# Kernel optimization log

Measured on AMD Instinct MI355X. Metric: run time of the kernel, lower is better.

Reference implementation:

```python
import jax, jax.numpy as jnp
import numpy as np
from functools import partial

B, T, D, H, V, L, NL = 2, 2048, 512, 8, 32000, 4, 3
HID = 4 * D
HD = D // H
EPS = 1e-5


def layernorm(x, g, b):
    mu = jnp.mean(x, axis=-1, keepdims=True)
    var = jnp.mean(jnp.square(x - mu), axis=-1, keepdims=True)
    return (x - mu) * jax.lax.rsqrt(var + EPS) * g + b


def self_mod_attn(x, Wq, Wk, Wv, Wo):
    # x: [B,T,D]; W*: [D,D] (applied as x @ W)
    def heads(w):
        return jnp.transpose((x @ w).reshape(B, T, H, HD), (1, 0, 2, 3))  # [T,B,H,HD]
    q, k, v = heads(Wq), heads(Wk), heads(Wv)

    def step(mem, qkv):
        q_t, k_t, v_t = qkv  # each [B,H,HD]
        mem = mem + jnp.einsum('bhd,bhk->hdk', v_t, k_t) / B  # batch-mean outer product
        y_t = jnp.einsum('hdk,bhk->bhd', mem, q_t)
        return mem, y_t

    mem0 = jnp.zeros((H, HD, HD), dtype=x.dtype)
    _, ys = jax.lax.scan(step, mem0, (q, k, v))  # ys: [T,B,H,HD]
    out = jnp.transpose(ys, (1, 0, 2, 3)).reshape(B, T, D)
    return out @ Wo


def cms(x, W1, b1, W2, b2):
    # Continuum memory system: NL parallel MLP levels (dim -> 4*dim -> dim, GELU), averaged.
    h = jax.nn.gelu(jnp.einsum('btd,ndh->nbth', x, W1) + b1[:, None, None, :])
    y = jnp.einsum('nbth,nhd->nbtd', h, W2) + b2[:, None, None, :]
    return jnp.mean(y, axis=0)


def setup_inputs() -> dict:
    key = jax.random.key(0)
    ks = jax.random.split(key, 16)
    std = 0.02
    p = {
        'emb': jax.random.normal(ks[0], (V, D), jnp.float32) * std,
        'pos': jax.random.normal(ks[1], (2048, D), jnp.float32) * std,
        'ln1_g': jnp.ones((L, D)), 'ln1_b': jnp.zeros((L, D)),
        'Wq': jax.random.normal(ks[2], (L, D, D), jnp.float32) * std,
        'Wk': jax.random.normal(ks[3], (L, D, D), jnp.float32) * std,
        'Wv': jax.random.normal(ks[4], (L, D, D), jnp.float32) * std,
        'Wo': jax.random.normal(ks[5], (L, D, D), jnp.float32) * std,
        'ln2_g': jnp.ones((L, D)), 'ln2_b': jnp.zeros((L, D)),
        'cms_W1': jax.random.normal(ks[6], (L, NL, D, HID), jnp.float32) * std,
        'cms_b1': jnp.zeros((L, NL, HID)),
        'cms_W2': jax.random.normal(ks[7], (L, NL, HID, D), jnp.float32) * std,
        'cms_b2': jnp.zeros((L, NL, D)),
        'lnf_g': jnp.ones((D,)), 'lnf_b': jnp.zeros((D,)),
        'input_ids': jax.random.randint(ks[8], (B, T), 0, V, jnp.int32),
    }
    return p


def reference(emb, pos, ln1_g, ln1_b, Wq, Wk, Wv, Wo, ln2_g, ln2_b,
              cms_W1, cms_b1, cms_W2, cms_b2, lnf_g, lnf_b, input_ids):
    x = emb[input_ids] + pos[:T][None, :, :]  # [B,T,D]
    for l in range(L):
        x = x + self_mod_attn(layernorm(x, ln1_g[l], ln1_b[l]), Wq[l], Wk[l], Wv[l], Wo[l])
        x = x + cms(layernorm(x, ln2_g[l], ln2_b[l]), cms_W1[l], cms_b1[l], cms_W2[l], cms_b2[l])
    x = layernorm(x, lnf_g, lnf_b)
    logits = x @ emb.T  # tied head, [B,T,V]
    return logits
```

## Files before the change

kernel.cpp:

```cpp
#include <hip/hip_runtime.h>
#include <stdint.h>

#define B_ 2
#define T_ 2048
#define D_ 512
#define H_ 8
#define HD_ 64
#define V_ 32000
#define L_ 4
#define NL_ 3
#define HID_ 2048
#define NROW 4096
#define CCH 64
#define CROWS 128
#define NC 32
#define EPS_ 1e-5f

typedef __attribute__((ext_vector_type(8))) __bf16 bf16x8;
typedef __attribute__((ext_vector_type(4))) float f32x4;

__device__ __forceinline__ float b2f(unsigned short u) {
  union { uint32_t i; float f; } v; v.i = ((uint32_t)u) << 16; return v.f;
}
__device__ __forceinline__ unsigned short f2b(float f) {
  union { float f; uint32_t i; } v; v.f = f;
  uint32_t u = v.i;
  u += 0x7fffu + ((u >> 16) & 1u);
  return (unsigned short)(u >> 16);
}

__global__ __launch_bounds__(256) void k_prep(
    const float* __restrict__ emb, const float* __restrict__ pos,
    const int* __restrict__ ids,
    const float* __restrict__ Wq, const float* __restrict__ Wk,
    const float* __restrict__ Wv, const float* __restrict__ Wo,
    const float* __restrict__ W1, const float* __restrict__ W2,
    const float* __restrict__ b2,
    const float* __restrict__ ln1g, const float* __restrict__ ln1b,
    unsigned short* __restrict__ WqkvT, unsigned short* __restrict__ WoT,
    unsigned short* __restrict__ W1T, unsigned short* __restrict__ W2cat,
    unsigned short* __restrict__ embB, float* __restrict__ bsum,
    float* __restrict__ x, unsigned short* __restrict__ h) {
  int bid = blockIdx.x, tid = threadIdx.x;
  __shared__ float tile[32][33];
  __shared__ float red[4], red2[4];
  int tx = tid & 31, ty = tid >> 5;
  if (bid < 4096) {
    int z = bid >> 8, r = bid & 255;
    int bx = (r & 15) * 32, by = (r >> 4) * 32;
    const float* in; unsigned short* out;
    if (z < 12) {
      int l = z / 3, m = z - l * 3;
      in = (m == 0 ? Wq : m == 1 ? Wk : Wv) + (size_t)l * D_ * D_;
      out = WqkvT + (size_t)z * D_ * D_;
    } else {
      in = Wo + (size_t)(z - 12) * D_ * D_;
      out = WoT + (size_t)(z - 12) * D_ * D_;
    }
#pragma unroll
    for (int i = 0; i < 4; i++)
      tile[ty + 8 * i][tx] = in[(size_t)(by + ty + 8 * i) * D_ + bx + tx];
    __syncthreads();
#pragma unroll
    for (int i = 0; i < 4; i++)
      out[(size_t)(bx + ty + 8 * i) * D_ + by + tx] = f2b(tile[tx][ty + 8 * i]);
  } else if (bid < 16384) {
    int s = bid - 4096;
    int z = s >> 10, r = s & 1023;
    int bx = (r & 63) * 32, by = (r >> 6) * 32;
    const float* in = W1 + (size_t)z * D_ * HID_;
    unsigned short* out = W1T + (size_t)z * HID_ * D_;
#pragma unroll
    for (int i = 0; i < 4; i++)
      tile[ty + 8 * i][tx] = in[(size_t)(by + ty + 8 * i) * HID_ + bx + tx];
    __syncthreads();
#pragma unroll
    for (int i = 0; i < 4; i++)
      out[(size_t)(bx + ty + 8 * i) * D_ + by + tx] = f2b(tile[tx][ty + 8 * i]);
  } else if (bid < 28672) {
    int s = bid - 16384;
    int z = s >> 10, r = s & 1023;
    int l = z / 3, n = z - l * 3;
    int bx = (r & 15) * 32, by = (r >> 4) * 32;
    const float* in = W2 + (size_t)z * HID_ * D_;
#pragma unroll
    for (int i = 0; i < 4; i++)
      tile[ty + 8 * i][tx] = in[(size_t)(by + ty + 8 * i) * D_ + bx + tx];
    __syncthreads();
#pragma unroll
    for (int i = 0; i < 4; i++)
      W2cat[((size_t)l * D_ + bx + ty + 8 * i) * (NL_ * HID_) + n * HID_ + by + tx] =
          f2b(tile[tx][ty + 8 * i]);
  } else if (bid < 44672) {
    int s = bid - 28672;
    int base = (s * 256 + tid) * 4;
    float4 v = *(const float4*)(emb + base);
    unsigned short o[4] = { f2b(v.x), f2b(v.y), f2b(v.z), f2b(v.w) };
    *(uint2*)(embB + base) = *(const uint2*)o;
  } else if (bid < 46720) {
    int s = bid - 44672;
    int i = s * 256 + tid;
    int row = i >> 7, cg = i & 127;
    int t = row & (T_ - 1);
    int id = ids[row];
    float4 e = ((const float4*)(emb + (size_t)id * D_))[cg];
    float4 p = ((const float4*)(pos + (size_t)t * D_))[cg];
    float4 xv; xv.x = e.x + p.x; xv.y = e.y + p.y; xv.z = e.z + p.z; xv.w = e.w + p.w;
    ((float4*)(x + (size_t)row * D_))[cg] = xv;
    float sum = xv.x + xv.y + xv.z + xv.w;
#pragma unroll
    for (int o = 32; o >= 1; o >>= 1) sum += __shfl_xor(sum, o);
    int wv = tid >> 6;
    if ((tid & 63) == 0) red[wv] = sum;
    __syncthreads();
    int wb = (tid >> 7) * 2;
    float mu = (red[wb] + red[wb + 1]) * (1.f / D_);
    float dx = xv.x - mu, dy = xv.y - mu, dz = xv.z - mu, dw = xv.w - mu;
    float s2 = dx * dx + dy * dy + dz * dz + dw * dw;
#pragma unroll
    for (int o = 32; o >= 1; o >>= 1) s2 += __shfl_xor(s2, o);
    if ((tid & 63) == 0) red2[wv] = s2;
    __syncthreads();
    float var = (red2[wb] + red2[wb + 1]) * (1.f / D_);
    float rs = rsqrtf(var + EPS_);
    float4 gv = ((const float4*)ln1g)[cg];
    float4 bv = ((const float4*)ln1b)[cg];
    unsigned short o4[4] = { f2b(dx * rs * gv.x + bv.x), f2b(dy * rs * gv.y + bv.y),
                             f2b(dz * rs * gv.z + bv.z), f2b(dw * rs * gv.w + bv.w) };
    *(uint2*)(h + (size_t)row * D_ + cg * 4) = *(const uint2*)o4;
  } else {
    int s = bid - 46720;
    int l = s >> 1, d = (s & 1) * 256 + tid;
    float acc = 0.f;
#pragma unroll
    for (int n = 0; n < NL_; n++) acc += b2[((size_t)l * NL_ + n) * D_ + d];
    bsum[(size_t)l * D_ + d] = acc;
  }
}

__global__ __launch_bounds__(128) void k_ln(
    const float* __restrict__ x, const float* __restrict__ g,
    const float* __restrict__ b, unsigned short* __restrict__ out) {
  int row = blockIdx.x;
  int tid = threadIdx.x;
  const float* xr = x + (size_t)row * D_;
  float4 v = ((const float4*)xr)[tid];
  float s = v.x + v.y + v.z + v.w;
#pragma unroll
  for (int o = 32; o >= 1; o >>= 1) s += __shfl_xor(s, o);
  __shared__ float red[2], red2[2];
  int wv = tid >> 6;
  if ((tid & 63) == 0) red[wv] = s;
  __syncthreads();
  float mu = (red[0] + red[1]) * (1.f / D_);
  float dx = v.x - mu, dy = v.y - mu, dz = v.z - mu, dw = v.w - mu;
  float s2 = dx * dx + dy * dy + dz * dz + dw * dw;
#pragma unroll
  for (int o = 32; o >= 1; o >>= 1) s2 += __shfl_xor(s2, o);
  if ((tid & 63) == 0) red2[wv] = s2;
  __syncthreads();
  float var = (red2[0] + red2[1]) * (1.f / D_);
  float rs = rsqrtf(var + EPS_);
  float4 gv = ((const float4*)g)[tid];
  float4 bv = ((const float4*)b)[tid];
  unsigned short o4[4] = { f2b(dx * rs * gv.x + bv.x), f2b(dy * rs * gv.y + bv.y),
                           f2b(dz * rs * gv.z + bv.z), f2b(dw * rs * gv.w + bv.w) };
  *(uint2*)(out + (size_t)row * D_ + tid * 4) = *(const uint2*)o4;
}

__global__ __launch_bounds__(256) void k_cmsred_ln(
    float* __restrict__ x, const float* __restrict__ parts,
    const float* __restrict__ bsum, const float* __restrict__ g,
    const float* __restrict__ b, unsigned short* __restrict__ h) {
  int bid = blockIdx.x, tid = threadIdx.x;
  int row = bid * 2 + (tid >> 7);
  int cg = tid & 127;
  size_t base = (size_t)row * D_ + cg * 4;
  float4 xv = *(const float4*)(x + base);
  float4 p0 = *(const float4*)(parts + base);
  float4 p1 = *(const float4*)(parts + (size_t)NROW * D_ + base);
  float4 p2 = *(const float4*)(parts + 2ull * NROW * D_ + base);
  float4 bs = *(const float4*)(bsum + cg * 4);
  const float k3 = 1.f / 3.f;
  xv.x += (p0.x + p1.x + p2.x + bs.x) * k3;
  xv.y += (p0.y + p1.y + p2.y + bs.y) * k3;
  xv.z += (p0.z + p1.z + p2.z + bs.z) * k3;
  xv.w += (p0.w + p1.w + p2.w + bs.w) * k3;
  *(float4*)(x + base) = xv;
  float sum = xv.x + xv.y + xv.z + xv.w;
#pragma unroll
  for (int o = 32; o >= 1; o >>= 1) sum += __shfl_xor(sum, o);
  __shared__ float red[4], red2[4];
  int wv = tid >> 6;
  if ((tid & 63) == 0) red[wv] = sum;
  __syncthreads();
  int wb = (tid >> 7) * 2;
  float mu = (red[wb] + red[wb + 1]) * (1.f / D_);
  float dx = xv.x - mu, dy = xv.y - mu, dz = xv.z - mu, dw = xv.w - mu;
  float s2 = dx * dx + dy * dy + dz * dz + dw * dw;
#pragma unroll
  for (int o = 32; o >= 1; o >>= 1) s2 += __shfl_xor(s2, o);
  if ((tid & 63) == 0) red2[wv] = s2;
  __syncthreads();
  float var = (red2[wb] + red2[wb + 1]) * (1.f / D_);
  float rs = rsqrtf(var + EPS_);
  float4 gv = ((const float4*)g)[cg];
  float4 bv = ((const float4*)b)[cg];
  unsigned short o4[4] = { f2b(dx * rs * gv.x + bv.x), f2b(dy * rs * gv.y + bv.y),
                           f2b(dz * rs * gv.z + bv.z), f2b(dw * rs * gv.w + bv.w) };
  *(uint2*)(h + base) = *(const uint2*)o4;
}

enum { E_QKV = 0, E_RES = 1, E_GELU = 2, E_PART = 3, E_F32 = 4 };

template <int TR, int NW>
__device__ __forceinline__ void stage_tile(
    const unsigned short* __restrict__ gbase, int ldk, unsigned short* lds,
    int wave, int lane) {
#pragma unroll
  for (int q = 0; q < 4; q++) {
    int Lb = (q * NW + wave) << 10;
    int L = Lb + lane * 16;
    int row = L >> 7;
    int colb = (L & 127) ^ ((row & 7) << 4);
    const unsigned short* gsrc = gbase + (size_t)row * ldk + (colb >> 1);
    __builtin_amdgcn_global_load_lds(
        (const __attribute__((address_space(1))) uint32_t*)gsrc,
        (__attribute__((address_space(3))) uint32_t*)(lds + (Lb >> 1)),
        16, 0, 0);
  }
}

template <int EPI>
__global__ __launch_bounds__(256, 2) void k_gemm128(
    const unsigned short* __restrict__ A,
    const unsigned short* __restrict__ Bt,
    const float* __restrict__ bias,
    void* __restrict__ Out,
    int Kext, int ldk, int N, int ldOut) {
  int z = blockIdx.z;
  A  += (size_t)z * Kext;
  Bt += (size_t)z * Kext;
  int lane = threadIdx.x & 63, wave = threadIdx.x >> 6;
  int wm = wave >> 1, wn = wave & 1;
  int bx = blockIdx.x, by = blockIdx.y;

  __shared__ __align__(16) unsigned short As[2][128 * 64];
  __shared__ __align__(16) unsigned short Bs[2][128 * 64];

  const unsigned short* Ab = A + (size_t)by * 128 * ldk;
  const unsigned short* Bb = Bt + (size_t)bx * 128 * ldk;

  f32x4 acc[4][4] = {};
  int nk = Kext / 64;
  stage_tile<128, 4>(Ab, ldk, As[0], wave, lane);
  stage_tile<128, 4>(Bb, ldk, Bs[0], wave, lane);
  __syncthreads();
  for (int kt = 0; kt < nk; kt++) {
    int cur = kt & 1;
    if (kt + 1 < nk) {
      stage_tile<128, 4>(Ab + (size_t)(kt + 1) * 64, ldk, As[cur ^ 1], wave, lane);
      stage_tile<128, 4>(Bb + (size_t)(kt + 1) * 64, ldk, Bs[cur ^ 1], wave, lane);
    }
    const char* Ac = (const char*)As[cur];
    const char* Bc = (const char*)Bs[cur];
#pragma unroll
    for (int kk = 0; kk < 2; kk++) {
      bf16x8 af[4], bfr[4];
#pragma unroll
      for (int mt = 0; mt < 4; mt++) {
        int row = wm * 64 + mt * 16 + (lane & 15);
        int off = ((row << 7) | (kk * 64 + ((lane >> 4) << 4))) ^ ((row & 7) << 4);
        af[mt] = *(const bf16x8*)(Ac + off);
      }
#pragma unroll
      for (int nt = 0; nt < 4; nt++) {
        int row = wn * 64 + nt * 16 + (lane & 15);
        int off = ((row << 7) | (kk * 64 + ((lane >> 4) << 4))) ^ ((row & 7) << 4);
        bfr[nt] = *(const bf16x8*)(Bc + off);
      }
#pragma unroll
      for (int mt = 0; mt < 4; mt++)
#pragma unroll
        for (int nt = 0; nt < 4; nt++)
          acc[mt][nt] = __builtin_amdgcn_mfma_f32_16x16x32_bf16(
              af[mt], bfr[nt], acc[mt][nt], 0, 0, 0);
    }
    __syncthreads();
  }

  int gm = by * 128 + wm * 64;
  int gn = bx * 128 + wn * 64;
#pragma unroll
  for (int mt = 0; mt < 4; mt++) {
#pragma unroll
    for (int nt = 0; nt < 4; nt++) {
      int m0 = gm + mt * 16 + ((lane >> 4) << 2);
      int n = gn + nt * 16 + (lane & 15);
#pragma unroll
      for (int j = 0; j < 4; j++) {
        float v = acc[mt][nt][j];
        int m = m0 + j;
        if constexpr (EPI == E_QKV) {
          int zq = n >> 9, col = n & 511;
          ((unsigned short*)Out)[((size_t)zq * NROW + m) * D_ + col] = f2b(v);
        } else if constexpr (EPI == E_RES) {
          size_t idx = (size_t)m * ldOut + n;
          ((float*)Out)[idx] = bias[idx] + v;
        } else {
          ((float*)Out)[(size_t)z * NROW * D_ + (size_t)m * ldOut + n] = v;
        }
      }
    }
  }
}

template <int EPI>
__global__ __launch_bounds__(512, 1) void k_gemm256(
    const unsigned short* __restrict__ A,
    const unsigned short* __restrict__ Bt,
    const float* __restrict__ bias,
    void* __restrict__ Out,
    int K, int N, int ldOut) {
  int lane = threadIdx.x & 63, wave = threadIdx.x >> 6;
  int wm = wave >> 2, wn = wave & 3;
  int bx = blockIdx.x, by = blockIdx.y;
  if constexpr (EPI == E_F32) {
    int lin = blockIdx.y * 125 + blockIdx.x;
    int seg = lin / 400, rem = lin % 400;
    bx = seg * 25 + rem % 25;  by = rem / 25;
  }

  __shared__ __align__(16) unsigned short As[2][256 * 64];
  __shared__ __align__(16) unsigned short Bs[2][256 * 64];

  const unsigned short* Ab = A + (size_t)by * 256 * K;
  const unsigned short* Bb = Bt + (size_t)bx * 256 * K;

  f32x4 acc[8][4] = {};
  int nk = K / 64;
  stage_tile<256, 8>(Ab, K, As[0], wave, lane);
  stage_tile<256, 8>(Bb, K, Bs[0], wave, lane);
  __syncthreads();
  for (int kt = 0; kt < nk; kt++) {
    int cur = kt & 1;
    if (kt + 1 < nk) {
      stage_tile<256, 8>(Ab + (size_t)(kt + 1) * 64, K, As[cur ^ 1], wave, lane);
      stage_tile<256, 8>(Bb + (size_t)(kt + 1) * 64, K, Bs[cur ^ 1], wave, lane);
    }
    const char* Ac = (const char*)As[cur];
    const char* Bc = (const char*)Bs[cur];
#pragma unroll
    for (int kk = 0; kk < 2; kk++) {
      bf16x8 af[8], bfr[4];
#pragma unroll
      for (int mt = 0; mt < 8; mt++) {
        int row = wm * 128 + mt * 16 + (lane & 15);
        int off = ((row << 7) | (kk * 64 + ((lane >> 4) << 4))) ^ ((row & 7) << 4);
        af[mt] = *(const bf16x8*)(Ac + off);
      }
#pragma unroll
      for (int nt = 0; nt < 4; nt++) {
        int row = wn * 64 + nt * 16 + (lane & 15);
        int off = ((row << 7) | (kk * 64 + ((lane >> 4) << 4))) ^ ((row & 7) << 4);
        bfr[nt] = *(const bf16x8*)(Bc + off);
      }
#pragma unroll
      for (int mt = 0; mt < 8; mt++)
#pragma unroll
        for (int nt = 0; nt < 4; nt++)
          acc[mt][nt] = __builtin_amdgcn_mfma_f32_16x16x32_bf16(
              af[mt], bfr[nt], acc[mt][nt], 0, 0, 0);
    }
    __syncthreads();
  }

  int gm = by * 256 + wm * 128;
  int gn = bx * 256 + wn * 64;
#pragma unroll
  for (int mt = 0; mt < 8; mt++) {
#pragma unroll
    for (int nt = 0; nt < 4; nt++) {
      int m0 = gm + mt * 16 + ((lane >> 4) << 2);
      int n = gn + nt * 16 + (lane & 15);
#pragma unroll
      for (int j = 0; j < 4; j++) {
        float v = acc[mt][nt][j];
        size_t idx = (size_t)(m0 + j) * ldOut + n;
        if constexpr (EPI == E_GELU) {
          v += bias[n];
          float u2 = 1.5957691216057308f * (v + 0.044715f * v * v * v);
          float sg = 1.f / (1.f + __expf(-u2));
          ((unsigned short*)Out)[idx] = f2b(v * sg);
        } else {
          ((float*)Out)[idx] = v;
        }
      }
    }
  }
}

__device__ __forceinline__ void unpack8f(uint4 u, float* dst) {
  dst[0] = b2f((unsigned short)(u.x & 0xffff)); dst[1] = b2f((unsigned short)(u.x >> 16));
  dst[2] = b2f((unsigned short)(u.y & 0xffff)); dst[3] = b2f((unsigned short)(u.y >> 16));
  dst[4] = b2f((unsigned short)(u.z & 0xffff)); dst[5] = b2f((unsigned short)(u.z >> 16));
  dst[6] = b2f((unsigned short)(u.w & 0xffff)); dst[7] = b2f((unsigned short)(u.w >> 16));
}

__global__ __launch_bounds__(256) void k_attnA(
    const unsigned short* __restrict__ kbuf, const unsigned short* __restrict__ vbuf,
    float* __restrict__ G) {
  int c = blockIdx.x, h = blockIdx.y;
  __shared__ __align__(16) float Ks[CROWS][HD_];
  __shared__ __align__(16) float Vs[CROWS][HD_];
  int tid = threadIdx.x;
#pragma unroll
  for (int it = 0; it < 4; it++) {
    int gi = it * 256 + tid;
    int r = gi >> 3, c8 = gi & 7;
    int bb = r & 1, tt = c * CCH + (r >> 1);
    size_t goff = ((size_t)bb * T_ + tt) * D_ + h * HD_ + c8 * 8;
    uint4 kv = *(const uint4*)(kbuf + goff);
    uint4 vv = *(const uint4*)(vbuf + goff);
    unpack8f(kv, &Ks[r][c8 * 8]);
    unpack8f(vv, &Vs[r][c8 * 8]);
  }
  __syncthreads();
  int d = tid & 63, kb = (tid >> 6) * 16;
  float acc[16] = {};
  for (int r = 0; r < CROWS; r++) {
    float vd = Vs[r][d];
    const float4* Kr = (const float4*)(&Ks[r][kb]);
    float4 k0 = Kr[0], k1 = Kr[1], k2 = Kr[2], k3 = Kr[3];
    acc[0] += vd * k0.x;  acc[1] += vd * k0.y;  acc[2] += vd * k0.z;  acc[3] += vd * k0.w;
    acc[4] += vd * k1.x;  acc[5] += vd * k1.y;  acc[6] += vd * k1.z;  acc[7] += vd * k1.w;
    acc[8] += vd * k2.x;  acc[9] += vd * k2.y;  acc[10] += vd * k2.z; acc[11] += vd * k2.w;
    acc[12] += vd * k3.x; acc[13] += vd * k3.y; acc[14] += vd * k3.z; acc[15] += vd * k3.w;
  }
  float* Gp = G + (((size_t)c * H_ + h) * HD_ + d) * HD_ + kb;
#pragma unroll
  for (int j = 0; j < 16; j++) Gp[j] = 0.5f * acc[j];
}

__global__ __launch_bounds__(256) void k_attnC(
    const unsigned short* __restrict__ qbuf, const unsigned short* __restrict__ kbuf,
    const unsigned short* __restrict__ vbuf, const float* __restrict__ G,
    unsigned short* __restrict__ ybuf) {
  int c = blockIdx.x, h = blockIdx.y;
  __shared__ __align__(16) unsigned short smem[32768];
  unsigned short* Qs  = smem;
  unsigned short* Ksh = smem + 8192;
  unsigned short* Vt  = smem + 16384;
  unsigned short* Mhi = smem + 24576;
  unsigned short* Mlo = smem + 28672;
  unsigned short* Ps  = smem;

  int tid = threadIdx.x, lane = tid & 63, w = tid >> 6;
  float macc[16] = {};
  for (int cp = 0; cp < c; cp++) {
    const float4* gp = (const float4*)(G + ((size_t)cp * H_ + h) * (HD_ * HD_)) + tid * 4;
#pragma unroll
    for (int j4 = 0; j4 < 4; j4++) {
      float4 gv = gp[j4];
      macc[j4 * 4]     += gv.x;
      macc[j4 * 4 + 1] += gv.y;
      macc[j4 * 4 + 2] += gv.z;
      macc[j4 * 4 + 3] += gv.w;
    }
  }
#pragma unroll
  for (int it = 0; it < 4; it++) {
    int gi = it * 256 + tid;
    int r = gi >> 3, g8 = gi & 7;
    int bb = r & 1, tt = c * CCH + (r >> 1);
    size_t go = ((size_t)bb * T_ + tt) * D_ + h * HD_ + g8 * 8;
    int qc = (g8 * 8) ^ ((r & 7) << 3);
    *(uint4*)(Qs + r * 64 + qc) = *(const uint4*)(qbuf + go);
    *(uint4*)(Ksh + r * 64 + qc) = *(const uint4*)(kbuf + go);
    uint4 vv = *(const uint4*)(vbuf + go);
    const unsigned short* vp = (const unsigned short*)&vv;
#pragma unroll
    for (int j = 0; j < 8; j++) {
      int d = g8 * 8 + j;
      int t = (d & 7) ^ (d >> 3);
      Vt[d * 128 + (r ^ (t << 3))] = vp[j];
    }
  }
#pragma unroll
  for (int j = 0; j < 16; j++) {
    int i = tid * 16 + j;
    int d = i >> 6, k = i & 63;
    unsigned short hi = f2b(macc[j]);
    float lo = macc[j] - b2f(hi);
    int col = k ^ ((d & 7) << 3);
    Mhi[d * 64 + col] = hi;
    Mlo[d * 64 + col] = f2b(lo);
  }
  __syncthreads();

  int row0 = w * 32;
  f32x4 sacc[2][8] = {};
  f32x4 yacc[2][4] = {};
#pragma unroll
  for (int kk = 0; kk < 2; kk++) {
    bf16x8 aq[2];
#pragma unroll
    for (int mt = 0; mt < 2; mt++) {
      int row = row0 + mt * 16 + (lane & 15);
      aq[mt] = *(const bf16x8*)(Qs + row * 64 +
                ((kk * 32 + ((lane >> 4) << 3)) ^ ((row & 7) << 3)));
    }
#pragma unroll
    for (int nt = 0; nt < 8; nt++) {
      int row = nt * 16 + (lane & 15);
      bf16x8 bk = *(const bf16x8*)(Ksh + row * 64 +
                ((kk * 32 + ((lane >> 4) << 3)) ^ ((row & 7) << 3)));
#pragma unroll
      for (int mt = 0; mt < 2; mt++)
        sacc[mt][nt] = __builtin_amdgcn_mfma_f32_16x16x32_bf16(aq[mt], bk,
                                                               sacc[mt][nt], 0, 0, 0);
    }
#pragma unroll
    for (int nt = 0; nt < 4; nt++) {
      int row = nt * 16 + (lane & 15);
      int off = row * 64 + ((kk * 32 + ((lane >> 4) << 3)) ^ ((row & 7) << 3));
      bf16x8 bh = *(const bf16x8*)(Mhi + off);
      bf16x8 bl = *(const bf16x8*)(Mlo + off);
#pragma unroll
      for (int mt = 0; mt < 2; mt++) {
        yacc[mt][nt] = __builtin_amdgcn_mfma_f32_16x16x32_bf16(aq[mt], bh,
                                                               yacc[mt][nt], 0, 0, 0);
        yacc[mt][nt] = __builtin_amdgcn_mfma_f32_16x16x32_bf16(aq[mt], bl,
                                                               yacc[mt][nt], 0, 0, 0);
      }
    }
  }
  __syncthreads();

#pragma unroll
  for (int mt = 0; mt < 2; mt++)
#pragma unroll
    for (int nt = 0; nt < 8; nt++)
#pragma unroll
      for (int j = 0; j < 4; j++) {
        int qr = row0 + mt * 16 + ((lane >> 4) << 2) + j;
        int ks = nt * 16 + (lane & 15);
        float v = ((ks >> 1) <= (qr >> 1)) ? sacc[mt][nt][j] * 0.5f : 0.f;
        Ps[qr * 128 + (ks ^ ((qr & 7) << 3))] = f2b(v);
      }
  __syncthreads();

  for (int kb = 0; kb <= w; kb++) {
    bf16x8 ap[2];
#pragma unroll
    for (int mt = 0; mt < 2; mt++) {
      int row = row0 + mt * 16 + (lane & 15);
      ap[mt] = *(const bf16x8*)(Ps + row * 128 +
                ((kb * 32 + ((lane >> 4) << 3)) ^ ((row & 7) << 3)));
    }
#pragma unroll
    for (int nt = 0; nt < 4; nt++) {
      int d = nt * 16 + (lane & 15);
      int t = (d & 7) ^ (d >> 3);
      int gb = (kb * 32 + ((lane >> 4) << 3)) ^ (t << 3);
      bf16x8 bv = *(const bf16x8*)(Vt + d * 128 + gb);
#pragma unroll
      for (int mt = 0; mt < 2; mt++)
        yacc[mt][nt] = __builtin_amdgcn_mfma_f32_16x16x32_bf16(ap[mt], bv,
                                                               yacc[mt][nt], 0, 0, 0);
    }
  }

#pragma unroll
  for (int mt = 0; mt < 2; mt++)
#pragma unroll
    for (int nt = 0; nt < 4; nt++)
#pragma unroll
      for (int j = 0; j < 4; j++) {
        int qr = row0 + mt * 16 + ((lane >> 4) << 2) + j;
        int d = nt * 16 + (lane & 15);
        int bb = qr & 1, tl = qr >> 1;
        ybuf[((size_t)bb * T_ + c * CCH + tl) * D_ + h * HD_ + d] =
            f2b(yacc[mt][nt][j]);
      }
}

extern "C" void kernel_launch(void* const* d_in, const int* in_sizes, int n_in,
                              void* d_out, int out_size, void* d_ws, size_t ws_size,
                              hipStream_t stream) {
  (void)in_sizes; (void)n_in; (void)out_size; (void)ws_size;
  const float* emb  = (const float*)d_in[0];
  const float* pos  = (const float*)d_in[1];
  const float* ln1g = (const float*)d_in[2];
  const float* ln1b = (const float*)d_in[3];
  const float* Wq   = (const float*)d_in[4];
  const float* Wk   = (const float*)d_in[5];
  const float* Wv   = (const float*)d_in[6];
  const float* Wo   = (const float*)d_in[7];
  const float* ln2g = (const float*)d_in[8];
  const float* ln2b = (const float*)d_in[9];
  const float* W1   = (const float*)d_in[10];
  const float* b1   = (const float*)d_in[11];
  const float* W2   = (const float*)d_in[12];
  const float* b2   = (const float*)d_in[13];
  const float* lnfg = (const float*)d_in[14];
  const float* lnfb = (const float*)d_in[15];
  const int*   ids  = (const int*)d_in[16];

  char* w = (char*)d_ws;
  size_t off = 0;
  auto alloc = [&](size_t bytes) -> void* {
    void* p = w + off; off += (bytes + 255) & ~(size_t)255; return p;
  };
  const size_t DD = (size_t)D_ * D_;
  unsigned short* WqkvT = (unsigned short*)alloc(12ull * DD * 2);
  unsigned short* WoT   = (unsigned short*)alloc(4ull * DD * 2);
  unsigned short* W1T   = (unsigned short*)alloc((size_t)L_ * NL_ * HID_ * D_ * 2);
  unsigned short* W2cat = (unsigned short*)alloc((size_t)L_ * D_ * NL_ * HID_ * 2);
  unsigned short* embB  = (unsigned short*)alloc((size_t)V_ * D_ * 2);
  float* bsum           = (float*)alloc((size_t)L_ * D_ * 4);
  float* x              = (float*)alloc((size_t)NROW * D_ * 4);
  unsigned short* h     = (unsigned short*)alloc((size_t)NROW * D_ * 2);
  unsigned short* qkv   = (unsigned short*)alloc(3ull * NROW * D_ * 2);
  unsigned short* ybuf  = (unsigned short*)alloc((size_t)NROW * D_ * 2);
  float* G              = (float*)alloc((size_t)NC * H_ * HD_ * HD_ * 4);
  (void)alloc((size_t)NC * H_ * HD_ * HD_ * 4);
  float* parts          = (float*)qkv;
  unsigned short* hmid  = (unsigned short*)alloc((size_t)NROW * NL_ * HID_ * 2);

  dim3 blk(256);
  k_prep<<<dim3(46728), blk, 0, stream>>>(emb, pos, ids, Wq, Wk, Wv, Wo, W1, W2, b2,
                                          ln1g, ln1b,
                                          WqkvT, WoT, W1T, W2cat, embB, bsum, x, h);

  unsigned short* qb = qkv;
  unsigned short* kb = qkv + (size_t)NROW * D_;
  unsigned short* vb = qkv + 2ull * NROW * D_;

  for (int l = 0; l < L_; l++) {
    k_gemm128<E_QKV><<<dim3(12, 32), blk, 0, stream>>>(
        h, WqkvT + (size_t)l * 3 * DD, bsum, qkv, D_, D_, 3 * D_, D_);
    k_attnA<<<dim3(NC, H_), blk, 0, stream>>>(kb, vb, G);
    k_attnC<<<dim3(NC, H_), blk, 0, stream>>>(qb, kb, vb, G, ybuf);
    k_gemm128<E_RES><<<dim3(4, 32), blk, 0, stream>>>(
        ybuf, WoT + (size_t)l * DD, x, x, D_, D_, D_, D_);
    k_ln<<<dim3(NROW), dim3(128), 0, stream>>>(x, ln2g + l * D_, ln2b + l * D_, h);
    k_gemm256<E_GELU><<<dim3(24, 16), dim3(512), 0, stream>>>(
        h, W1T + (size_t)l * NL_ * HID_ * D_, b1 + (size_t)l * NL_ * HID_, hmid,
        D_, NL_ * HID_, NL_ * HID_);
    k_gemm128<E_PART><<<dim3(4, 32, 3), blk, 0, stream>>>(
        hmid, W2cat + (size_t)l * D_ * NL_ * HID_, bsum, parts,
        2048, NL_ * HID_, D_, D_);
    const float* gn = (l < 3) ? (ln1g + (l + 1) * D_) : lnfg;
    const float* bn = (l < 3) ? (ln1b + (l + 1) * D_) : lnfb;
    k_cmsred_ln<<<dim3(NROW / 2), blk, 0, stream>>>(x, parts, bsum + l * D_, gn, bn, h);
  }
  k_gemm256<E_F32><<<dim3(125, 16), dim3(512), 0, stream>>>(
      h, embB, bsum, d_out, D_, V_, V_);
}
```

Measured before the change: 972.8 us.

## Fuse attention kernels with atomic grid barrier and single-buffer big GEMM LDS

Merges the two attention kernels (per-chunk K^T V state build and the chunked output pass) into one launch. A per-layer, per-head atomic counter, zeroed in the prep kernel, acts as a cross-block barrier so each block waits for all chunk states before building its prefix memory. Q/K/V staging for the second phase is issued before the spin so it overlaps the wait. Separately, the 256-tile GEMM drops LDS double buffering and its min-1-block launch bound, halving shared memory to allow more resident blocks at the cost of losing load/compute overlap. The spin barrier relies on all 256 blocks being co-resident.

```diff
diff --git a/kernel.cpp b/kernel.cpp
--- a/kernel.cpp
+++ b/kernel.cpp
@@ -40,7 +40,8 @@
     unsigned short* __restrict__ WqkvT, unsigned short* __restrict__ WoT,
     unsigned short* __restrict__ W1T, unsigned short* __restrict__ W2cat,
     unsigned short* __restrict__ embB, float* __restrict__ bsum,
-    float* __restrict__ x, unsigned short* __restrict__ h) {
+    float* __restrict__ x, unsigned short* __restrict__ h,
+    int* __restrict__ cnt) {
   int bid = blockIdx.x, tid = threadIdx.x;
   __shared__ float tile[32][33];
   __shared__ float red[4], red2[4];
@@ -128,13 +129,15 @@
     unsigned short o4[4] = { f2b(dx * rs * gv.x + bv.x), f2b(dy * rs * gv.y + bv.y),
                              f2b(dz * rs * gv.z + bv.z), f2b(dw * rs * gv.w + bv.w) };
     *(uint2*)(h + (size_t)row * D_ + cg * 4) = *(const uint2*)o4;
-  } else {
+  } else if (bid < 46728) {
     int s = bid - 46720;
     int l = s >> 1, d = (s & 1) * 256 + tid;
     float acc = 0.f;
 #pragma unroll
     for (int n = 0; n < NL_; n++) acc += b2[((size_t)l * NL_ + n) * D_ + d];
     bsum[(size_t)l * D_ + d] = acc;
+  } else {
+    if (tid < L_ * H_) cnt[tid] = 0;
   }
 }
 
@@ -316,7 +319,7 @@
 }
 
 template <int EPI>
-__global__ __launch_bounds__(512, 1) void k_gemm256(
+__global__ __launch_bounds__(512) void k_gemm256(
     const unsigned short* __restrict__ A,
     const unsigned short* __restrict__ Bt,
     const float* __restrict__ bias,
@@ -331,25 +334,20 @@
     bx = seg * 25 + rem % 25;  by = rem / 25;
   }
 
-  __shared__ __align__(16) unsigned short As[2][256 * 64];
-  __shared__ __align__(16) unsigned short Bs[2][256 * 64];
+  __shared__ __align__(16) unsigned short As[256 * 64];
+  __shared__ __align__(16) unsigned short Bs[256 * 64];
 
   const unsigned short* Ab = A + (size_t)by * 256 * K;
   const unsigned short* Bb = Bt + (size_t)bx * 256 * K;
 
   f32x4 acc[8][4] = {};
   int nk = K / 64;
-  stage_tile<256, 8>(Ab, K, As[0], wave, lane);
-  stage_tile<256, 8>(Bb, K, Bs[0], wave, lane);
-  __syncthreads();
   for (int kt = 0; kt < nk; kt++) {
-    int cur = kt & 1;
-    if (kt + 1 < nk) {
-      stage_tile<256, 8>(Ab + (size_t)(kt + 1) * 64, K, As[cur ^ 1], wave, lane);
-      stage_tile<256, 8>(Bb + (size_t)(kt + 1) * 64, K, Bs[cur ^ 1], wave, lane);
-    }
-    const char* Ac = (const char*)As[cur];
-    const char* Bc = (const char*)Bs[cur];
+    stage_tile<256, 8>(Ab + (size_t)kt * 64, K, As, wave, lane);
+    stage_tile<256, 8>(Bb + (size_t)kt * 64, K, Bs, wave, lane);
+    __syncthreads();
+    const char* Ac = (const char*)As;
+    const char* Bc = (const char*)Bs;
 #pragma unroll
     for (int kk = 0; kk < 2; kk++) {
       bf16x8 af[8], bfr[4];
@@ -407,67 +405,57 @@
   dst[6] = b2f((unsigned short)(u.w & 0xffff)); dst[7] = b2f((unsigned short)(u.w >> 16));
 }
 
-__global__ __launch_bounds__(256) void k_attnA(
-    const unsigned short* __restrict__ kbuf, const unsigned short* __restrict__ vbuf,
-    float* __restrict__ G) {
+__global__ __launch_bounds__(256) void k_attn(
+    const unsigned short* __restrict__ qbuf, const unsigned short* __restrict__ kbuf,
+    const unsigned short* __restrict__ vbuf, float* __restrict__ G,
+    int* __restrict__ cnt, unsigned short* __restrict__ ybuf) {
   int c = blockIdx.x, h = blockIdx.y;
-  __shared__ __align__(16) float Ks[CROWS][HD_];
-  __shared__ __align__(16) float Vs[CROWS][HD_];
-  int tid = threadIdx.x;
-#pragma unroll
-  for (int it = 0; it < 4; it++) {
-    int gi = it * 256 + tid;
-    int r = gi >> 3, c8 = gi & 7;
-    int bb = r & 1, tt = c * CCH + (r >> 1);
-    size_t goff = ((size_t)bb * T_ + tt) * D_ + h * HD_ + c8 * 8;
-    uint4 kv = *(const uint4*)(kbuf + goff);
-    uint4 vv = *(const uint4*)(vbuf + goff);
-    unpack8f(kv, &Ks[r][c8 * 8]);
-    unpack8f(vv, &Vs[r][c8 * 8]);
-  }
-  __syncthreads();
-  int d = tid & 63, kb = (tid >> 6) * 16;
-  float acc[16] = {};
-  for (int r = 0; r < CROWS; r++) {
-    float vd = Vs[r][d];
-    const float4* Kr = (const float4*)(&Ks[r][kb]);
-    float4 k0 = Kr[0], k1 = Kr[1], k2 = Kr[2], k3 = Kr[3];
-    acc[0] += vd * k0.x;  acc[1] += vd * k0.y;  acc[2] += vd * k0.z;  acc[3] += vd * k0.w;
-    acc[4] += vd * k1.x;  acc[5] += vd * k1.y;  acc[6] += vd * k1.z;  acc[7] += vd * k1.w;
-    acc[8] += vd * k2.x;  acc[9] += vd * k2.y;  acc[10] += vd * k2.z; acc[11] += vd * k2.w;
-    acc[12] += vd * k3.x; acc[13] += vd * k3.y; acc[14] += vd * k3.z; acc[15] += vd * k3.w;
-  }
-  float* Gp = G + (((size_t)c * H_ + h) * HD_ + d) * HD_ + kb;
-#pragma unroll
-  for (int j = 0; j < 16; j++) Gp[j] = 0.5f * acc[j];
-}
-
-__global__ __launch_bounds__(256) void k_attnC(
-    const unsigned short* __restrict__ qbuf, const unsigned short* __restrict__ kbuf,
-    const unsigned short* __restrict__ vbuf, const float* __restrict__ G,
-    unsigned short* __restrict__ ybuf) {
-  int c = blockIdx.x, h = blockIdx.y;
-  __shared__ __align__(16) unsigned short smem[32768];
+  __shared__ __align__(16) char sm_raw[65536];
+  int tid = threadIdx.x, lane = tid & 63, w = tid >> 6;
+
+  {
+    float (*Ks)[HD_] = (float(*)[HD_])sm_raw;
+    float (*Vs)[HD_] = (float(*)[HD_])(sm_raw + 32768);
+#pragma unroll
+    for (int it = 0; it < 4; it++) {
+      int gi = it * 256 + tid;
+      int r = gi >> 3, c8 = gi & 7;
+      int bb = r & 1, tt = c * CCH + (r >> 1);
+      size_t goff = ((size_t)bb * T_ + tt) * D_ + h * HD_ + c8 * 8;
+      uint4 kv = *(const uint4*)(kbuf + goff);
+      uint4 vv = *(const uint4*)(vbuf + goff);
+      unpack8f(kv, &Ks[r][c8 * 8]);
+      unpack8f(vv, &Vs[r][c8 * 8]);
+    }
+    __syncthreads();
+    int d = tid & 63, kb = (tid >> 6) * 16;
+    float acc[16] = {};
+    for (int r = 0; r < CROWS; r++) {
+      float vd = Vs[r][d];
+      const float4* Kr = (const float4*)(&Ks[r][kb]);
+      float4 k0 = Kr[0], k1 = Kr[1], k2 = Kr[2], k3 = Kr[3];
+      acc[0] += vd * k0.x;  acc[1] += vd * k0.y;  acc[2] += vd * k0.z;  acc[3] += vd * k0.w;
+      acc[4] += vd * k1.x;  acc[5] += vd * k1.y;  acc[6] += vd * k1.z;  acc[7] += vd * k1.w;
+      acc[8] += vd * k2.x;  acc[9] += vd * k2.y;  acc[10] += vd * k2.z; acc[11] += vd * k2.w;
+      acc[12] += vd * k3.x; acc[13] += vd * k3.y; acc[14] += vd * k3.z; acc[15] += vd * k3.w;
+    }
+    float* Gp = G + (((size_t)c * H_ + h) * HD_ + d) * HD_ + kb;
+#pragma unroll
+    for (int j = 0; j < 16; j++) Gp[j] = 0.5f * acc[j];
+    __syncthreads();
+    if (tid == 0) {
+      __threadfence();
+      __hip_atomic_fetch_add(&cnt[h], 1, __ATOMIC_RELEASE, __HIP_MEMORY_SCOPE_AGENT);
+    }
+  }
+
+  unsigned short* smem = (unsigned short*)sm_raw;
   unsigned short* Qs  = smem;
   unsigned short* Ksh = smem + 8192;
   unsigned short* Vt  = smem + 16384;
   unsigned short* Mhi = smem + 24576;
   unsigned short* Mlo = smem + 28672;
   unsigned short* Ps  = smem;
-
-  int tid = threadIdx.x, lane = tid & 63, w = tid >> 6;
-  float macc[16] = {};
-  for (int cp = 0; cp < c; cp++) {
-    const float4* gp = (const float4*)(G + ((size_t)cp * H_ + h) * (HD_ * HD_)) + tid * 4;
-#pragma unroll
-    for (int j4 = 0; j4 < 4; j4++) {
-      float4 gv = gp[j4];
-      macc[j4 * 4]     += gv.x;
-      macc[j4 * 4 + 1] += gv.y;
-      macc[j4 * 4 + 2] += gv.z;
-      macc[j4 * 4 + 3] += gv.w;
-    }
-  }
 #pragma unroll
   for (int it = 0; it < 4; it++) {
     int gi = it * 256 + tid;
@@ -484,6 +472,25 @@
       int d = g8 * 8 + j;
       int t = (d & 7) ^ (d >> 3);
       Vt[d * 128 + (r ^ (t << 3))] = vp[j];
+    }
+  }
+
+  if (tid == 0) {
+    while (__hip_atomic_load(&cnt[h], __ATOMIC_ACQUIRE, __HIP_MEMORY_SCOPE_AGENT) < NC) {}
+    __threadfence();
+  }
+  __syncthreads();
+
+  float macc[16] = {};
+  for (int cp = 0; cp < c; cp++) {
+    const float4* gp = (const float4*)(G + ((size_t)cp * H_ + h) * (HD_ * HD_)) + tid * 4;
+#pragma unroll
+    for (int j4 = 0; j4 < 4; j4++) {
+      float4 gv = gp[j4];
+      macc[j4 * 4]     += gv.x;
+      macc[j4 * 4 + 1] += gv.y;
+      macc[j4 * 4 + 2] += gv.z;
+      macc[j4 * 4 + 3] += gv.w;
     }
   }
 #pragma unroll
@@ -619,6 +626,7 @@
   unsigned short* W2cat = (unsigned short*)alloc((size_t)L_ * D_ * NL_ * HID_ * 2);
   unsigned short* embB  = (unsigned short*)alloc((size_t)V_ * D_ * 2);
   float* bsum           = (float*)alloc((size_t)L_ * D_ * 4);
+  int*   cnt            = (int*)alloc((size_t)L_ * H_ * 4);
   float* x              = (float*)alloc((size_t)NROW * D_ * 4);
   unsigned short* h     = (unsigned short*)alloc((size_t)NROW * D_ * 2);
   unsigned short* qkv   = (unsigned short*)alloc(3ull * NROW * D_ * 2);
@@ -629,9 +637,10 @@
   unsigned short* hmid  = (unsigned short*)alloc((size_t)NROW * NL_ * HID_ * 2);
 
   dim3 blk(256);
-  k_prep<<<dim3(46728), blk, 0, stream>>>(emb, pos, ids, Wq, Wk, Wv, Wo, W1, W2, b2,
+  k_prep<<<dim3(46729), blk, 0, stream>>>(emb, pos, ids, Wq, Wk, Wv, Wo, W1, W2, b2,
                                           ln1g, ln1b,
-                                          WqkvT, WoT, W1T, W2cat, embB, bsum, x, h);
+                                          WqkvT, WoT, W1T, W2cat, embB, bsum, x, h,
+                                          cnt);
 
   unsigned short* qb = qkv;
   unsigned short* kb = qkv + (size_t)NROW * D_;
@@ -640,8 +649,7 @@
   for (int l = 0; l < L_; l++) {
     k_gemm128<E_QKV><<<dim3(12, 32), blk, 0, stream>>>(
         h, WqkvT + (size_t)l * 3 * DD, bsum, qkv, D_, D_, 3 * D_, D_);
-    k_attnA<<<dim3(NC, H_), blk, 0, stream>>>(kb, vb, G);
-    k_attnC<<<dim3(NC, H_), blk, 0, stream>>>(qb, kb, vb, G, ybuf);
+    k_attn<<<dim3(NC, H_), blk, 0, stream>>>(qb, kb, vb, G, cnt + l * H_, ybuf);
     k_gemm128<E_RES><<<dim3(4, 32), blk, 0, stream>>>(
         ybuf, WoT + (size_t)l * DD, x, x, D_, D_, D_, D_);
     k_ln<<<dim3(NROW), dim3(128), 0, stream>>>(x, ln2g + l * D_, ln2b + l * D_, h);
```

Measured after the change: 1.135 ms. +16.7%, slower.
